# Performance work log

Hardware: AMD Instinct MI355X
Metric: run time of the kernel (lower is better)

The kernel has to match this reference:

```python
import jax, jax.numpy as jnp
import numpy as np

N = 16384
E = 262144
NODE_DIM = 120
NUM_HEADS = 4
NUM_BASIS = 20
MULS = (64, 32, 16)          # multiplicities of 0e, 1e, 2e
LS = (0, 1, 2)
NUM_IRREPS = 112             # 64+32+16
EQUI_DIM = 240               # 64*1 + 32*3 + 16*5
L_MAX = 2
ATTN_DIM_SCALAR = NODE_DIM // NUM_HEADS        # 30
ATTN_DIM_EQUI = NODE_DIM // (L_MAX + 1)        # 40
SCALE_SCALAR = 1.0 / np.sqrt(NODE_DIM)
SCALE_EQUI = 1.0 / np.sqrt(NUM_IRREPS)
EPS = 1e-5

def _blocks():
    off = 0
    for mul, l in zip(MULS, LS):
        d = 2 * l + 1
        yield off, mul, l, d
        off += mul * d

def equi_dot(x):
    # per-irrep self dot: [E, EQUI_DIM] -> [E, NUM_IRREPS] invariants
    outs = []
    for off, mul, l, d in _blocks():
        blk = x[:, off:off + mul * d].reshape(-1, mul, d)
        outs.append(jnp.sum(blk * blk, axis=-1))
    return jnp.concatenate(outs, axis=1)

def gate_to_components(g):
    # broadcast per-irrep scalar gate [E, NUM_IRREPS] to components [E, EQUI_DIM]
    parts = []
    woff = 0
    for mul, l in zip(MULS, LS):
        d = 2 * l + 1
        parts.append(jnp.repeat(g[:, woff:woff + mul, None], d, axis=-1).reshape(-1, mul * d))
        woff += mul
    return jnp.concatenate(parts, axis=1)

def layer_norm(x, w, b):
    mu = jnp.mean(x, -1, keepdims=True)
    var = jnp.var(x, -1, keepdims=True)
    return (x - mu) * jax.lax.rsqrt(var + EPS) * w + b

def o3_layer_norm(x, w):
    # equivariant layer norm: per irrep block, RMS over (mul, components); mean-center l=0 only
    parts = []
    woff = 0
    for off, mul, l, d in _blocks():
        blk = x[:, off:off + mul * d].reshape(-1, mul, d)
        if l == 0:
            blk = blk - jnp.mean(blk, axis=1, keepdims=True)
        rms = jax.lax.rsqrt(jnp.mean(blk * blk, axis=(1, 2), keepdims=True) + EPS)
        blk = blk * rms * w[woff:woff + mul][None, :, None]
        parts.append(blk.reshape(-1, mul * d))
        woff += mul
    return jnp.concatenate(parts, axis=1)

def mlp(x, w1, b1, w2, b2):
    return jax.nn.silu(x @ w1 + b1) @ w2 + b2

def setup_inputs():
    ks = jax.random.split(jax.random.key(0), 24)
    def lin(k, i, o):
        return jax.random.normal(k, (i, o), jnp.float32) / np.sqrt(i)
    return dict(
        node_scalar=jax.random.normal(ks[0], (N, NODE_DIM), jnp.float32),
        node_equi=jax.random.normal(ks[1], (N, EQUI_DIM), jnp.float32),
        rbf=jax.random.normal(ks[2], (E, NUM_BASIS), jnp.float32),
        fcut=jax.random.uniform(ks[3], (E, 1), jnp.float32),
        rsh=jax.random.normal(ks[4], (E, EQUI_DIM), jnp.float32),
        ln_w=jnp.ones((NODE_DIM,), jnp.float32),
        ln_b=jnp.zeros((NODE_DIM,), jnp.float32),
        o3ln_w=jnp.ones((NUM_IRREPS,), jnp.float32),
        Wq=lin(ks[5], NODE_DIM, NODE_DIM),
        Wk=lin(ks[6], NODE_DIM, NODE_DIM),
        Wv=lin(ks[7], NODE_DIM, NODE_DIM),
        Wqs=lin(ks[8], NODE_DIM, NODE_DIM),
        Wks=lin(ks[9], NODE_DIM, NODE_DIM),
        Wvs=lin(ks[10], NODE_DIM, NUM_IRREPS),
        rbf_w1=lin(ks[11], NUM_BASIS, NODE_DIM),
        rbf_b1=jnp.zeros((NODE_DIM,), jnp.float32),
        rbf_w2=lin(ks[12], NODE_DIM, NODE_DIM),
        rbf_b2=jnp.zeros((NODE_DIM,), jnp.float32),
        inv_w1=lin(ks[13], NUM_IRREPS, NODE_DIM),
        inv_b1=jnp.zeros((NODE_DIM,), jnp.float32),
        inv_w2=lin(ks[14], NODE_DIM, NODE_DIM),
        inv_b2=jnp.zeros((NODE_DIM,), jnp.float32),
        edge_index=jax.random.randint(ks[15], (2, E), 0, N),
    )

def reference(node_scalar, node_equi, rbf, fcut, rsh, ln_w, ln_b, o3ln_w, Wq, Wk, Wv, Wqs, Wks, Wvs, rbf_w1, rbf_b1, rbf_w2, rbf_b2, inv_w1, inv_b1, inv_w2, inv_b2, edge_index):
    center, neighbor = edge_index[0], edge_index[1]
    ns = layer_norm(node_scalar, ln_w, ln_b)
    ne = o3_layer_norm(node_equi, o3ln_w)
    q_inv = ns @ Wq; k_inv = ns @ Wk; v_inv = ns @ Wv
    q_sph = ns @ Wqs; k_sph = ns @ Wks; v_sph = ns @ Wvs
    # EquiFilter: equivariant difference -> per-irrep invariants -> MLP, plus radial MLP
    x_ij = ne[neighbor] - ne[center]
    w_ij = mlp(equi_dot(x_ij), inv_w1, inv_b1, inv_w2, inv_b2) + mlp(rbf, rbf_w1, rbf_b1, rbf_w2, rbf_b2)
    w_ij = w_ij * fcut
    # scalar multi-head dot-product attention (softmax-free)
    q_s = (q_inv[center] * w_ij).reshape(E, NUM_HEADS, ATTN_DIM_SCALAR)
    k_s = k_inv[neighbor].reshape(E, NUM_HEADS, ATTN_DIM_SCALAR)
    v_s = v_inv[neighbor].reshape(E, NUM_HEADS, ATTN_DIM_SCALAR)
    attn_s = jnp.sum(q_s * k_s, -1, keepdims=True) * SCALE_SCALAR
    msg_scalar = (attn_s * v_s).reshape(E, NODE_DIM)
    # equivariant gated attention
    q_e = (q_sph[center] * w_ij).reshape(E, L_MAX + 1, ATTN_DIM_EQUI)
    k_e = k_sph[neighbor].reshape(E, L_MAX + 1, ATTN_DIM_EQUI)
    v_e = v_sph[neighbor]                                   # [E, NUM_IRREPS]
    attn_e = jnp.sum(q_e * k_e, -1) * SCALE_EQUI            # [E, L_MAX+1]
    attn_e = jnp.concatenate([jnp.repeat(attn_e[:, i:i + 1], MULS[i], axis=1) for i in range(L_MAX + 1)], axis=1)
    gate = attn_e * v_e                                     # [E, NUM_IRREPS]
    msg_equi = rsh * gate_to_components(gate) * fcut        # elementwise tensor product with 0e gates
    out_scalar = node_scalar.at[center].add(msg_scalar)
    out_equi = node_equi.at[center].add(msg_equi)
    return out_scalar, out_equi
```

## Files before the change

kernel.cpp:

```cpp
#include <hip/hip_runtime.h>
#include <hip/hip_bf16.h>
#include <hip/hip_fp16.h>

#define N_NODES 16384
#define E_EDGES 262144

#define SCALE_S 0.09128709291752768f
#define SCALE_E 0.09449111825230679f

#define OFF_ACC   256
#define ACC_BYTES ((size_t)N_NODES * 360 * 4)
#define OFF_TAB   (OFF_ACC + ACC_BYTES)
#define OFF_NS    (OFF_TAB + (size_t)N_NODES * 952 * 2)
#define OFF_W1T   (OFF_NS + (size_t)N_NODES * 128 * 2)
#define OFF_W2T   (OFF_W1T + 256 * 160 * 2)
#define OFF_WNT   (OFF_W2T + 128 * 256 * 2)
#define OFF_B1    (OFF_WNT + 768 * 128 * 2)
#define OFF_B2    (OFF_B1 + 1024)
#define OFF_WIJ   (OFF_B2 + 512)

#define OFF_CNT   OFF_ACC
#define OFF_BASE  (OFF_ACC + 65536)
#define OFF_CUR   (OFF_ACC + 131584)
#define OFF_SORT  (OFF_ACC + 197632)
#define SORT_CLR_BYTES 197632

typedef __attribute__((ext_vector_type(8))) short short8;
typedef __attribute__((ext_vector_type(4))) float f32x4;

#define SF_STRIDE 168
#define SB_STRIDE 40
#define TR_STRIDE 40

#define REGION1_BYTES (64 * 240 * 2)
#define SMEM_MLP (64 * SF_STRIDE * 2 + REGION1_BYTES + 64 * 4 + 2 * 64 * 4)

static __device__ __forceinline__ float b2f(short s) {
    return __uint_as_float(((unsigned int)(unsigned short)s) << 16);
}
static __device__ __forceinline__ short f2b(float v) {
    __hip_bfloat16 h = __float2bfloat16(v);
    return *reinterpret_cast<short*>(&h);
}
static __device__ __forceinline__ short f2h(float v) {
    __half h = __float2half(v);
    return *reinterpret_cast<short*>(&h);
}
static __device__ __forceinline__ float h2f(short s) {
    __half h = *reinterpret_cast<__half*>(&s);
    return __half2float(h);
}
static __device__ __forceinline__ float ldin(const void* p, size_t i, int bfm) {
    return bfm ? b2f(((const short*)p)[i]) : ((const float*)p)[i];
}
static __device__ __forceinline__ float block_reduce(float v, float* red, int t) {
    __syncthreads();
    red[t] = v;
    __syncthreads();
    for (int s = 128; s > 0; s >>= 1) {
        if (t < s) red[t] += red[t + s];
        __syncthreads();
    }
    return red[0];
}

__global__ void detect_kernel(const unsigned short* __restrict__ lnw_bits, int* __restrict__ flag) {
    if (threadIdx.x == 0 && blockIdx.x == 0)
        *flag = (lnw_bits[0] == 0x3F80u) ? 1 : 0;
}

__global__ __launch_bounds__(256) void hist_kernel(const int* __restrict__ eidx, void* ws) {
    int* cnt = (int*)((char*)ws + OFF_CNT);
    int e = blockIdx.x * 256 + threadIdx.x;
    atomicAdd(&cnt[eidx[e]], 1);
}

__global__ __launch_bounds__(256) void scan_kernel(void* ws) {
    __shared__ int lds[256];
    int* cnt  = (int*)((char*)ws + OFF_CNT);
    int* base = (int*)((char*)ws + OFF_BASE);
    const int t = threadIdx.x;
    int s = 0;
    for (int j = 0; j < 64; ++j) s += cnt[t * 64 + j];
    lds[t] = s;
    __syncthreads();
    for (int off = 1; off < 256; off <<= 1) {
        int add = (t >= off) ? lds[t - off] : 0;
        __syncthreads();
        lds[t] += add;
        __syncthreads();
    }
    int run = lds[t] - s;
    for (int j = 0; j < 64; ++j) {
        int v = cnt[t * 64 + j];
        base[t * 64 + j] = run;
        run += v;
    }
    if (t == 0) base[16384] = E_EDGES;
}

__global__ __launch_bounds__(256) void scatter_kernel(const int* __restrict__ eidx, void* ws) {
    const int* base = (const int*)((char*)ws + OFF_BASE);
    int* cur    = (int*)((char*)ws + OFF_CUR);
    int* sorted = (int*)((char*)ws + OFF_SORT);
    int e = blockIdx.x * 256 + threadIdx.x;
    int c = eidx[e];
    int pos = base[c] + atomicAdd(&cur[c], 1);
    sorted[pos] = e;
}

__global__ __launch_bounds__(256) void prep_kernel(
    const void* inv_w1, const void* rbf_w1, const void* inv_w2, const void* rbf_w2,
    const void* inv_b1, const void* rbf_b1, const void* inv_b2, const void* rbf_b2,
    const void* Wq, const void* Wk, const void* Wv,
    const void* Wqs, const void* Wks, const void* Wvs,
    void* ws, const int* __restrict__ flag)
{
    short* W1T = (short*)((char*)ws + OFF_W1T);
    short* W2T = (short*)((char*)ws + OFF_W2T);
    short* WNT = (short*)((char*)ws + OFF_WNT);
    float* b1c = (float*)((char*)ws + OFF_B1);
    float* b2c = (float*)((char*)ws + OFF_B2);
    const int bfm = *flag;
    int g = blockIdx.x * 256 + threadIdx.x;
    if (g < 40960) {
        int n = g / 160, k = g % 160;
        float v = 0.f;
        if (n < 120 && k < 112) v = ldin(inv_w1, (size_t)k * 120 + n, bfm);
        else if (n >= 120 && n < 240 && k >= 112 && k < 132)
            v = ldin(rbf_w1, (size_t)(k - 112) * 120 + (n - 120), bfm);
        W1T[g] = f2b(v);
    } else if (g < 73728) {
        int g2 = g - 40960;
        int n = g2 / 256, k = g2 % 256;
        float v = 0.f;
        if (n < 120) {
            if (k < 120)      v = ldin(inv_w2, (size_t)k * 120 + n, bfm);
            else if (k < 240) v = ldin(rbf_w2, (size_t)(k - 120) * 120 + n, bfm);
        }
        W2T[g2] = f2b(v);
    } else if (g < 172032) {
        int g3 = g - 73728;
        int n = g3 / 128, k = g3 % 128;
        float v = 0.f;
        if (k < 120) {
            if      (n < 120) v = ldin(Wq,  (size_t)k * 120 + n, bfm);
            else if (n < 240) v = ldin(Wk,  (size_t)k * 120 + (n - 120), bfm);
            else if (n < 360) v = ldin(Wv,  (size_t)k * 120 + (n - 240), bfm);
            else if (n < 480) v = ldin(Wqs, (size_t)k * 120 + (n - 360), bfm);
            else if (n < 600) v = ldin(Wks, (size_t)k * 120 + (n - 480), bfm);
            else if (n < 712) v = ldin(Wvs, (size_t)k * 112 + (n - 600), bfm);
        }
        WNT[g3] = f2b(v);
    } else if (g < 172288) {
        int n = g - 172032;
        b1c[n] = (n < 120) ? ldin(inv_b1, n, bfm) : (n < 240 ? ldin(rbf_b1, n - 120, bfm) : 0.f);
    } else if (g < 172416) {
        int n = g - 172288;
        b2c[n] = (n < 120) ? (ldin(inv_b2, n, bfm) + ldin(rbf_b2, n, bfm)) : 0.f;
    }
}

__global__ __launch_bounds__(256) void nodeln_kernel(
    const void* node_scalar, const void* node_equi,
    const void* ln_w, const void* ln_b, const void* o3ln_w,
    void* ws, const int* __restrict__ flag)
{
    __shared__ float red[256];
    short* NS  = (short*)((char*)ws + OFF_NS);
    short* tab = (short*)((char*)ws + OFF_TAB);
    const int n = blockIdx.x, t = threadIdx.x;
    const int bfm = *flag;

    float xs = 0.f;
    if (t < 120) xs = ldin(node_scalar, (size_t)n * 120 + t, bfm);
    float s  = block_reduce(xs, red, t);
    float s2 = block_reduce(xs * xs, red, t);
    float mean = s * (1.f / 120.f);
    float var  = s2 * (1.f / 120.f) - mean * mean;
    float rstd = rsqrtf(var + 1e-5f);
    float nsv = 0.f;
    if (t < 120) nsv = (xs - mean) * rstd * ldin(ln_w, t, bfm) + ldin(ln_b, t, bfm);
    if (t < 128) NS[(size_t)n * 128 + t] = f2b(t < 120 ? nsv : 0.f);

    float xe = 0.f;
    if (t < 240) xe = ldin(node_equi, (size_t)n * 240 + t, bfm);
    float s0  = block_reduce(t < 64 ? xe : 0.f, red, t);
    float mu0 = s0 * (1.f / 64.f);
    float xc  = (t < 64) ? xe - mu0 : xe;
    float ss0 = block_reduce(t < 64 ? xc * xc : 0.f, red, t);
    float ss1 = block_reduce((t >= 64 && t < 160) ? xe * xe : 0.f, red, t);
    float ss2 = block_reduce((t >= 160 && t < 240) ? xe * xe : 0.f, red, t);
    float r0 = rsqrtf(ss0 * (1.f / 64.f) + 1e-5f);
    float r1 = rsqrtf(ss1 * (1.f / 96.f) + 1e-5f);
    float r2 = rsqrtf(ss2 * (1.f / 80.f) + 1e-5f);
    float nev = 0.f;
    if (t < 64)       nev = xc * r0 * ldin(o3ln_w, t, bfm);
    else if (t < 160) nev = xe * r1 * ldin(o3ln_w, 64 + (t - 64) / 3, bfm);
    else if (t < 240) nev = xe * r2 * ldin(o3ln_w, 96 + (t - 160) / 5, bfm);
    if (t < 240) tab[(size_t)n * 952 + 712 + t] = f2b(nev);
}

__global__ __launch_bounds__(256) void gemm_node_kernel(void* ws)
{
    __shared__ short sA[64 * SB_STRIDE];
    __shared__ short sB[64 * SB_STRIDE];
    const short* NS  = (const short*)((char*)ws + OFF_NS);
    const short* WNT = (const short*)((char*)ws + OFF_WNT);
    short* tab = (short*)((char*)ws + OFF_TAB);

    const int t = threadIdx.x, w = t >> 6, lane = t & 63;
    const int quad = lane >> 4, l15 = lane & 15;
    const int tileM = (blockIdx.x & 255) * 64;
    const int tileN = (blockIdx.x >> 8) * 64;

    f32x4 acc[4];
    for (int i = 0; i < 4; ++i) acc[i] = (f32x4){0.f, 0.f, 0.f, 0.f};

    for (int k0 = 0; k0 < 128; k0 += 32) {
        __syncthreads();
        {
            int row = t >> 2, ch = t & 3;
            *(short8*)&sA[row * SB_STRIDE + ch * 8] =
                *(const short8*)&NS[(size_t)(tileM + row) * 128 + k0 + ch * 8];
            *(short8*)&sB[row * SB_STRIDE + ch * 8] =
                *(const short8*)&WNT[(size_t)(tileN + row) * 128 + k0 + ch * 8];
        }
        __syncthreads();
        short8 a = *(const short8*)&sA[(w * 16 + l15) * SB_STRIDE + quad * 8];
        #pragma unroll
        for (int nt = 0; nt < 4; ++nt) {
            short8 b = *(const short8*)&sB[(nt * 16 + l15) * SB_STRIDE + quad * 8];
            acc[nt] = __builtin_amdgcn_mfma_f32_16x16x32_bf16(a, b, acc[nt], 0, 0, 0);
        }
    }
    #pragma unroll
    for (int nt = 0; nt < 4; ++nt)
        #pragma unroll
        for (int r = 0; r < 4; ++r) {
            int row = tileM + w * 16 + quad * 4 + r;
            int col = tileN + nt * 16 + l15;
            if (col < 712) tab[(size_t)row * 952 + col] = f2b(acc[nt][r]);
        }
}

__global__ __launch_bounds__(256, 3) void mlp_kernel(
    const void* rbf, const void* fcut, const int* __restrict__ eidx,
    void* ws, const int* __restrict__ flag)
{
    extern __shared__ __align__(16) char smem[];
    short* sF   = (short*)smem;
    char*  reg1 = smem + 64 * SF_STRIDE * 2;
    short* sD   = (short*)reg1;
    short* sB   = (short*)reg1;
    short* sTr  = (short*)(reg1 + 256 * SB_STRIDE * 2);
    float* sFc  = (float*)(reg1 + REGION1_BYTES);
    int*   sIC  = (int*)(sFc + 64);
    int*   sIN  = sIC + 64;

    const short* tab = (const short*)((char*)ws + OFF_TAB);
    const short* W1T = (const short*)((char*)ws + OFF_W1T);
    const short* W2T = (const short*)((char*)ws + OFF_W2T);
    const float* b1c = (const float*)((char*)ws + OFF_B1);
    const float* b2c = (const float*)((char*)ws + OFF_B2);
    short* Wij = (short*)((char*)ws + OFF_WIJ);

    const int t = threadIdx.x, w = t >> 6, lane = t & 63;
    const int quad = lane >> 4, l15 = lane & 15;
    const int bfm = *flag;
    const int e0 = blockIdx.x * 64;

    if (t < 64)       sIC[t] = eidx[e0 + t];
    else if (t < 128) sIN[t - 64] = eidx[E_EDGES + e0 + (t - 64)];
    else if (t < 192) sFc[t - 128] = ldin(fcut, e0 + (t - 128), bfm);
    __syncthreads();

    for (int u = t; u < 1920; u += 256) {
        int le = u / 30, ch = u - le * 30;
        const short* pc = tab + (size_t)sIC[le] * 952 + 712 + ch * 8;
        const short* pn = tab + (size_t)sIN[le] * 952 + 712 + ch * 8;
        short8 a = *(const short8*)pc;
        short8 b = *(const short8*)pn;
        short8 s;
        #pragma unroll
        for (int j = 0; j < 8; ++j) {
            float d = b2f(b[j]) - b2f(a[j]);
            s[j] = f2h(d * d);
        }
        *(short8*)&sD[le * 240 + ch * 8] = s;
    }
    __syncthreads();

    for (int u = t; u < 8192; u += 256) {
        int le = u >> 7, ir = u & 127;
        if (ir < 112) {
            const short* p = sD + le * 240;
            float a;
            if (ir < 64) {
                a = h2f(p[ir]);
            } else if (ir < 96) {
                int off = 64 + 3 * (ir - 64);
                a = h2f(p[off]) + h2f(p[off + 1]) + h2f(p[off + 2]);
            } else {
                int off = 160 + 5 * (ir - 96);
                a = h2f(p[off]) + h2f(p[off + 1]) + h2f(p[off + 2])
                  + h2f(p[off + 3]) + h2f(p[off + 4]);
            }
            sF[le * SF_STRIDE + ir] = f2b(a);
        }
    }
    for (int u = t; u < 4096; u += 256) {
        int le = u >> 6, c = u & 63;
        if (c < 48) {
            float v = (c < 20) ? ldin(rbf, (size_t)(e0 + le) * 20 + c, bfm) : 0.f;
            sF[le * SF_STRIDE + 112 + c] = f2b(v);
        }
    }
    __syncthreads();

    f32x4 acc[16];
    #pragma unroll
    for (int i = 0; i < 16; ++i) acc[i] = (f32x4){0.f, 0.f, 0.f, 0.f};
    for (int k0 = 0; k0 < 160; k0 += 32) {
        #pragma unroll
        for (int i = 0; i < 4; ++i) {
            int u = t + i * 256, n = u >> 2, ch = u & 3;
            *(short8*)&sB[n * SB_STRIDE + ch * 8] =
                *(const short8*)&W1T[(size_t)n * 160 + k0 + ch * 8];
        }
        __syncthreads();
        short8 a = *(const short8*)&sF[(w * 16 + l15) * SF_STRIDE + k0 + quad * 8];
        #pragma unroll
        for (int nt = 0; nt < 16; ++nt) {
            short8 b = *(const short8*)&sB[(nt * 16 + l15) * SB_STRIDE + quad * 8];
            acc[nt] = __builtin_amdgcn_mfma_f32_16x16x32_bf16(a, b, acc[nt], 0, 0, 0);
        }
        __syncthreads();
    }

    short* trw = sTr + w * (16 * TR_STRIDE);
    f32x4 acc2[8];
    #pragma unroll
    for (int i = 0; i < 8; ++i) acc2[i] = (f32x4){0.f, 0.f, 0.f, 0.f};
    #pragma unroll
    for (int ks = 0; ks < 8; ++ks) {
        #pragma unroll
        for (int h = 0; h < 2; ++h) {
            int nt = 2 * ks + h;
            float bb = b1c[nt * 16 + l15];
            #pragma unroll
            for (int r = 0; r < 4; ++r) {
                float v = acc[nt][r] + bb;
                v = v / (1.f + __expf(-v));
                trw[(quad * 4 + r) * TR_STRIDE + h * 16 + l15] = f2b(v);
            }
        }
        #pragma unroll
        for (int i = 0; i < 2; ++i) {
            int u = t + i * 256, n = u >> 2, ch = u & 3;
            *(short8*)&sB[n * SB_STRIDE + ch * 8] =
                *(const short8*)&W2T[(size_t)n * 256 + ks * 32 + ch * 8];
        }
        __syncthreads();
        short8 a = *(const short8*)&trw[l15 * TR_STRIDE + quad * 8];
        #pragma unroll
        for (int nt = 0; nt < 8; ++nt) {
            short8 b = *(const short8*)&sB[(nt * 16 + l15) * SB_STRIDE + quad * 8];
            acc2[nt] = __builtin_amdgcn_mfma_f32_16x16x32_bf16(a, b, acc2[nt], 0, 0, 0);
        }
        __syncthreads();
    }

    #pragma unroll
    for (int nt = 0; nt < 8; ++nt)
        #pragma unroll
        for (int r = 0; r < 4; ++r) {
            int lrow = w * 16 + quad * 4 + r;
            int col = nt * 16 + l15;
            float v = (acc2[nt][r] + b2c[col]) * sFc[lrow];
            Wij[(size_t)(e0 + lrow) * 128 + col] = f2b(v);
        }
}

__global__ __launch_bounds__(256) void edge2g_kernel(
    const void* node_scalar, const void* node_equi,
    const void* rsh, const void* fcut, const int* __restrict__ eidx,
    void* ws, void* out, const int* __restrict__ flag)
{
    const short* tab = (const short*)((char*)ws + OFF_TAB);
    const short* Wij = (const short*)((char*)ws + OFF_WIJ);
    const int* base   = (const int*)((char*)ws + OFF_BASE);
    const int* sorted = (const int*)((char*)ws + OFF_SORT);

    const int t = threadIdx.x, wvid = t >> 6, lane = t & 63;
    const int c = blockIdx.x * 4 + wvid;
    const int bfm = *flag;
    const short* tc = tab + (size_t)c * 952;

    const int i16 = lane & 15, g = lane >> 4;
    const int ksa = 30 * g + i16;
    const bool vb = (i16 < 14);
    const int ksb = ksa + 16;
    const int kea = 40 * g + i16;
    const bool ge = (g < 3), gec = ge && (i16 < 8);
    const float qs_a = b2f(tc[ksa]);
    const float qs_b = vb ? b2f(tc[ksb]) : 0.f;
    const float qe_a = ge  ? b2f(tc[360 + kea])      : 0.f;
    const float qe_b = ge  ? b2f(tc[360 + kea + 16]) : 0.f;
    const float qe_c = gec ? b2f(tc[360 + kea + 32]) : 0.f;
    const int bs0 = 16 * (lane / 30);
    const int bs1 = 16 * ((lane + 64) / 30);
    int wi_[4], be_[4];
    bool jv_[4];
    #pragma unroll
    for (int s = 0; s < 4; ++s) {
        int j = lane + 64 * s;
        jv_[s] = (j < 240);
        int wi = 0, le = 0;
        if (j < 64)       { wi = j;                  le = 0; }
        else if (j < 160) { wi = 64 + (j - 64) / 3;  le = 1; }
        else if (j < 240) { wi = 96 + (j - 160) / 5; le = 2; }
        wi_[s] = wi; be_[s] = 16 * le;
    }

    float accS0 = 0.f, accS1 = 0.f;
    float accE0 = 0.f, accE1 = 0.f, accE2 = 0.f, accE3 = 0.f;

    const int b0 = base[c], b1 = base[c + 1];
    for (int p = b0; p < b1; ++p) {
        const int e = sorted[p];
        const int n = eidx[E_EDGES + e];
        const short* tn = tab + (size_t)n * 952;
        const short* wr = Wij + (size_t)e * 128;
        const float fc = ldin(fcut, e, bfm);

        float ps = qs_a * b2f(wr[ksa]) * b2f(tn[120 + ksa])
                 + qs_b * b2f(wr[ksb]) * b2f(tn[120 + ksb]);
        float wv_ea = ge  ? b2f(wr[kea])      : 0.f;
        float wv_eb = ge  ? b2f(wr[kea + 16]) : 0.f;
        float wv_ec = gec ? b2f(wr[kea + 32]) : 0.f;
        float pe = qe_a * wv_ea * b2f(tn[480 + kea])
                 + qe_b * wv_eb * b2f(tn[480 + kea + 16])
                 + qe_c * wv_ec * b2f(tn[480 + kea + 32]);
        #pragma unroll
        for (int m = 1; m < 16; m <<= 1) {
            ps += __shfl_xor(ps, m, 16);
            pe += __shfl_xor(pe, m, 16);
        }
        ps *= SCALE_S;
        pe *= SCALE_E;

        float a0 = __shfl(ps, bs0);
        float a1 = __shfl(ps, bs1);
        accS0 += a0 * b2f(tn[240 + lane]);
        if (lane < 56) accS1 += a1 * b2f(tn[240 + 64 + lane]);

        float ae0 = __shfl(pe, be_[0]);
        float ae1 = __shfl(pe, be_[1]);
        float ae2 = __shfl(pe, be_[2]);
        float ae3 = __shfl(pe, be_[3]);
        accE0 += ae0 * b2f(tn[600 + wi_[0]]) * ldin(rsh, (size_t)e * 240 + lane, bfm) * fc;
        accE1 += ae1 * b2f(tn[600 + wi_[1]]) * ldin(rsh, (size_t)e * 240 + lane + 64, bfm) * fc;
        accE2 += ae2 * b2f(tn[600 + wi_[2]]) * ldin(rsh, (size_t)e * 240 + lane + 128, bfm) * fc;
        if (jv_[3])
            accE3 += ae3 * b2f(tn[600 + wi_[3]]) * ldin(rsh, (size_t)e * 240 + lane + 192, bfm) * fc;
    }

    const size_t so = (size_t)c * 120;
    {
        float v = ldin(node_scalar, so + lane, bfm) + accS0;
        size_t i = so + lane;
        if (bfm) ((short*)out)[i] = f2b(v); else ((float*)out)[i] = v;
    }
    if (lane < 56) {
        float v = ldin(node_scalar, so + 64 + lane, bfm) + accS1;
        size_t i = so + 64 + lane;
        if (bfm) ((short*)out)[i] = f2b(v); else ((float*)out)[i] = v;
    }
    const size_t eo = (size_t)c * 240;
    const size_t ob = (size_t)N_NODES * 120;
    {
        float v = ldin(node_equi, eo + lane, bfm) + accE0;
        size_t i = ob + eo + lane;
        if (bfm) ((short*)out)[i] = f2b(v); else ((float*)out)[i] = v;
    }
    {
        float v = ldin(node_equi, eo + lane + 64, bfm) + accE1;
        size_t i = ob + eo + lane + 64;
        if (bfm) ((short*)out)[i] = f2b(v); else ((float*)out)[i] = v;
    }
    {
        float v = ldin(node_equi, eo + lane + 128, bfm) + accE2;
        size_t i = ob + eo + lane + 128;
        if (bfm) ((short*)out)[i] = f2b(v); else ((float*)out)[i] = v;
    }
    if (jv_[3]) {
        float v = ldin(node_equi, eo + lane + 192, bfm) + accE3;
        size_t i = ob + eo + lane + 192;
        if (bfm) ((short*)out)[i] = f2b(v); else ((float*)out)[i] = v;
    }
}

extern "C" void kernel_launch(void* const* d_in, const int* in_sizes, int n_in,
                              void* d_out, int out_size, void* d_ws, size_t ws_size,
                              hipStream_t stream) {
    const void* node_scalar = d_in[0];
    const void* node_equi   = d_in[1];
    const void* rbf         = d_in[2];
    const void* fcut        = d_in[3];
    const void* rsh         = d_in[4];
    const void* ln_w        = d_in[5];
    const void* ln_b        = d_in[6];
    const void* o3ln_w      = d_in[7];
    const void* Wq          = d_in[8];
    const void* Wk          = d_in[9];
    const void* Wv          = d_in[10];
    const void* Wqs         = d_in[11];
    const void* Wks         = d_in[12];
    const void* Wvs         = d_in[13];
    const void* rbf_w1      = d_in[14];
    const void* rbf_b1      = d_in[15];
    const void* rbf_w2      = d_in[16];
    const void* rbf_b2      = d_in[17];
    const void* inv_w1      = d_in[18];
    const void* inv_b1      = d_in[19];
    const void* inv_w2      = d_in[20];
    const void* inv_b2      = d_in[21];
    const int*  edge_index  = (const int*)d_in[22];

    int* flag = (int*)d_ws;

    hipFuncSetAttribute(reinterpret_cast<const void*>(mlp_kernel),
                        hipFuncAttributeMaxDynamicSharedMemorySize, SMEM_MLP);

    detect_kernel<<<1, 64, 0, stream>>>((const unsigned short*)ln_w, flag);
    hipMemsetAsync((char*)d_ws + OFF_ACC, 0, SORT_CLR_BYTES, stream);

    hist_kernel<<<E_EDGES / 256, 256, 0, stream>>>(edge_index, d_ws);
    scan_kernel<<<1, 256, 0, stream>>>(d_ws);
    scatter_kernel<<<E_EDGES / 256, 256, 0, stream>>>(edge_index, d_ws);

    prep_kernel<<<674, 256, 0, stream>>>(
        inv_w1, rbf_w1, inv_w2, rbf_w2, inv_b1, rbf_b1, inv_b2, rbf_b2,
        Wq, Wk, Wv, Wqs, Wks, Wvs, d_ws, flag);

    nodeln_kernel<<<N_NODES, 256, 0, stream>>>(
        node_scalar, node_equi, ln_w, ln_b, o3ln_w, d_ws, flag);

    gemm_node_kernel<<<256 * 12, 256, 0, stream>>>(d_ws);

    mlp_kernel<<<E_EDGES / 64, 256, SMEM_MLP, stream>>>(
        rbf, fcut, edge_index, d_ws, flag);

    edge2g_kernel<<<N_NODES / 4, 256, 0, stream>>>(
        node_scalar, node_equi, rsh, fcut, edge_index, d_ws, d_out, flag);
}
```

Before: 847.8 us.

## Software-pipeline edge gather loads and use wave-shuffle reductions in node layernorm

The edge aggregation loop now double-buffers per-edge operands in registers. It issues the gathers for the next edge (Wij row, neighbor table entries, rsh, fcut) before computing the current edge, which hides gather latency behind the shuffle-reduction math. The node layer-norm kernel replaces repeated shared-memory tree reductions, each with many barriers, with wave-level xor-shuffle reductions that batch three sums at a time and need only two block barriers. The cost is higher register pressure from the two ER buffers, which may reduce occupancy.

```diff
diff --git a/kernel.cpp b/kernel.cpp
--- a/kernel.cpp
+++ b/kernel.cpp
@@ -52,16 +52,6 @@
 }
 static __device__ __forceinline__ float ldin(const void* p, size_t i, int bfm) {
     return bfm ? b2f(((const short*)p)[i]) : ((const float*)p)[i];
-}
-static __device__ __forceinline__ float block_reduce(float v, float* red, int t) {
-    __syncthreads();
-    red[t] = v;
-    __syncthreads();
-    for (int s = 128; s > 0; s >>= 1) {
-        if (t < s) red[t] += red[t + s];
-        __syncthreads();
-    }
-    return red[0];
 }
 
 __global__ void detect_kernel(const unsigned short* __restrict__ lnw_bits, int* __restrict__ flag) {
@@ -166,31 +156,54 @@
     const void* ln_w, const void* ln_b, const void* o3ln_w,
     void* ws, const int* __restrict__ flag)
 {
-    __shared__ float red[256];
+    __shared__ float sm[24];
     short* NS  = (short*)((char*)ws + OFF_NS);
     short* tab = (short*)((char*)ws + OFF_TAB);
-    const int n = blockIdx.x, t = threadIdx.x;
+    const int n = blockIdx.x, t = threadIdx.x, wv = t >> 6, lane = t & 63;
     const int bfm = *flag;
 
-    float xs = 0.f;
-    if (t < 120) xs = ldin(node_scalar, (size_t)n * 120 + t, bfm);
-    float s  = block_reduce(xs, red, t);
-    float s2 = block_reduce(xs * xs, red, t);
+    float xs = (t < 120) ? ldin(node_scalar, (size_t)n * 120 + t, bfm) : 0.f;
+    float xe = (t < 240) ? ldin(node_equi, (size_t)n * 240 + t, bfm) : 0.f;
+
+    float a = xs, b = xs * xs, c = (t < 64) ? xe : 0.f;
+    #pragma unroll
+    for (int m = 1; m < 64; m <<= 1) {
+        a += __shfl_xor(a, m);
+        b += __shfl_xor(b, m);
+        c += __shfl_xor(c, m);
+    }
+    if (lane == 0) { sm[wv * 3] = a; sm[wv * 3 + 1] = b; sm[wv * 3 + 2] = c; }
+    __syncthreads();
+    float s  = sm[0] + sm[3] + sm[6] + sm[9];
+    float s2 = sm[1] + sm[4] + sm[7] + sm[10];
+    float s0 = sm[2] + sm[5] + sm[8] + sm[11];
+
     float mean = s * (1.f / 120.f);
     float var  = s2 * (1.f / 120.f) - mean * mean;
     float rstd = rsqrtf(var + 1e-5f);
-    float nsv = 0.f;
-    if (t < 120) nsv = (xs - mean) * rstd * ldin(ln_w, t, bfm) + ldin(ln_b, t, bfm);
-    if (t < 128) NS[(size_t)n * 128 + t] = f2b(t < 120 ? nsv : 0.f);
-
-    float xe = 0.f;
-    if (t < 240) xe = ldin(node_equi, (size_t)n * 240 + t, bfm);
-    float s0  = block_reduce(t < 64 ? xe : 0.f, red, t);
+    if (t < 128) {
+        float nsv = 0.f;
+        if (t < 120) nsv = (xs - mean) * rstd * ldin(ln_w, t, bfm) + ldin(ln_b, t, bfm);
+        NS[(size_t)n * 128 + t] = f2b(nsv);
+    }
+
     float mu0 = s0 * (1.f / 64.f);
     float xc  = (t < 64) ? xe - mu0 : xe;
-    float ss0 = block_reduce(t < 64 ? xc * xc : 0.f, red, t);
-    float ss1 = block_reduce((t >= 64 && t < 160) ? xe * xe : 0.f, red, t);
-    float ss2 = block_reduce((t >= 160 && t < 240) ? xe * xe : 0.f, red, t);
+    float p0 = (t < 64) ? xc * xc : 0.f;
+    float p1 = (t >= 64 && t < 160) ? xe * xe : 0.f;
+    float p2 = (t >= 160 && t < 240) ? xe * xe : 0.f;
+    #pragma unroll
+    for (int m = 1; m < 64; m <<= 1) {
+        p0 += __shfl_xor(p0, m);
+        p1 += __shfl_xor(p1, m);
+        p2 += __shfl_xor(p2, m);
+    }
+    if (lane == 0) { sm[12 + wv * 3] = p0; sm[12 + wv * 3 + 1] = p1; sm[12 + wv * 3 + 2] = p2; }
+    __syncthreads();
+    float ss0 = sm[12] + sm[15] + sm[18] + sm[21];
+    float ss1 = sm[13] + sm[16] + sm[19] + sm[22];
+    float ss2 = sm[14] + sm[17] + sm[20] + sm[23];
+
     float r0 = rsqrtf(ss0 * (1.f / 64.f) + 1e-5f);
     float r1 = rsqrtf(ss1 * (1.f / 96.f) + 1e-5f);
     float r2 = rsqrtf(ss2 * (1.f / 80.f) + 1e-5f);
@@ -382,6 +395,13 @@
         }
 }
 
+struct ER {
+    float wsa, wsb, wea, web, wec;
+    float ka, kb, kae, kbe, kce;
+    float v0, v1, vs0, vs1, vs2, vs3;
+    float r0, r1, r2, r3, fc;
+};
+
 __global__ __launch_bounds__(256) void edge2g_kernel(
     const void* node_scalar, const void* node_equi,
     const void* rsh, const void* fcut, const int* __restrict__ eidx,
@@ -410,12 +430,11 @@
     const float qe_c = gec ? b2f(tc[360 + kea + 32]) : 0.f;
     const int bs0 = 16 * (lane / 30);
     const int bs1 = 16 * ((lane + 64) / 30);
+    const bool jv3 = (lane < 48);
     int wi_[4], be_[4];
-    bool jv_[4];
     #pragma unroll
     for (int s = 0; s < 4; ++s) {
         int j = lane + 64 * s;
-        jv_[s] = (j < 240);
         int wi = 0, le = 0;
         if (j < 64)       { wi = j;                  le = 0; }
         else if (j < 160) { wi = 64 + (j - 64) / 3;  le = 1; }
@@ -426,22 +445,37 @@
     float accS0 = 0.f, accS1 = 0.f;
     float accE0 = 0.f, accE1 = 0.f, accE2 = 0.f, accE3 = 0.f;
 
-    const int b0 = base[c], b1 = base[c + 1];
-    for (int p = b0; p < b1; ++p) {
-        const int e = sorted[p];
-        const int n = eidx[E_EDGES + e];
-        const short* tn = tab + (size_t)n * 952;
+    auto loadE = [&](ER& R, int e, int nn) {
+        const short* tn = tab + (size_t)nn * 952;
         const short* wr = Wij + (size_t)e * 128;
-        const float fc = ldin(fcut, e, bfm);
-
-        float ps = qs_a * b2f(wr[ksa]) * b2f(tn[120 + ksa])
-                 + qs_b * b2f(wr[ksb]) * b2f(tn[120 + ksb]);
-        float wv_ea = ge  ? b2f(wr[kea])      : 0.f;
-        float wv_eb = ge  ? b2f(wr[kea + 16]) : 0.f;
-        float wv_ec = gec ? b2f(wr[kea + 32]) : 0.f;
-        float pe = qe_a * wv_ea * b2f(tn[480 + kea])
-                 + qe_b * wv_eb * b2f(tn[480 + kea + 16])
-                 + qe_c * wv_ec * b2f(tn[480 + kea + 32]);
+        R.wsa = b2f(wr[ksa]);
+        R.wsb = b2f(wr[ksb]);
+        R.ka  = b2f(tn[120 + ksa]);
+        R.kb  = b2f(tn[120 + ksb]);
+        if (ge) {
+            R.wea = b2f(wr[kea]);
+            R.web = b2f(wr[kea + 16]);
+            R.wec = b2f(wr[kea + 32]);
+        } else { R.wea = 0.f; R.web = 0.f; R.wec = 0.f; }
+        R.kae = b2f(tn[480 + kea]);
+        R.kbe = b2f(tn[480 + kea + 16]);
+        R.kce = b2f(tn[480 + kea + 32]);
+        R.v0  = b2f(tn[240 + lane]);
+        R.v1  = b2f(tn[304 + lane]);
+        R.vs0 = b2f(tn[600 + wi_[0]]);
+        R.vs1 = b2f(tn[600 + wi_[1]]);
+        R.vs2 = b2f(tn[600 + wi_[2]]);
+        R.vs3 = b2f(tn[600 + wi_[3]]);
+        R.r0  = ldin(rsh, (size_t)e * 240 + lane, bfm);
+        R.r1  = ldin(rsh, (size_t)e * 240 + lane + 64, bfm);
+        R.r2  = ldin(rsh, (size_t)e * 240 + lane + 128, bfm);
+        R.r3  = jv3 ? ldin(rsh, (size_t)e * 240 + lane + 192, bfm) : 0.f;
+        R.fc  = ldin(fcut, e, bfm);
+    };
+
+    auto computeE = [&](const ER& R) {
+        float ps = qs_a * R.wsa * R.ka + qs_b * R.wsb * R.kb;
+        float pe = qe_a * R.wea * R.kae + qe_b * R.web * R.kbe + qe_c * R.wec * R.kce;
         #pragma unroll
         for (int m = 1; m < 16; m <<= 1) {
             ps += __shfl_xor(ps, m, 16);
@@ -449,21 +483,34 @@
         }
         ps *= SCALE_S;
         pe *= SCALE_E;
-
-        float a0 = __shfl(ps, bs0);
-        float a1 = __shfl(ps, bs1);
-        accS0 += a0 * b2f(tn[240 + lane]);
-        if (lane < 56) accS1 += a1 * b2f(tn[240 + 64 + lane]);
-
+        float a0  = __shfl(ps, bs0);
+        float a1  = __shfl(ps, bs1);
         float ae0 = __shfl(pe, be_[0]);
         float ae1 = __shfl(pe, be_[1]);
         float ae2 = __shfl(pe, be_[2]);
         float ae3 = __shfl(pe, be_[3]);
-        accE0 += ae0 * b2f(tn[600 + wi_[0]]) * ldin(rsh, (size_t)e * 240 + lane, bfm) * fc;
-        accE1 += ae1 * b2f(tn[600 + wi_[1]]) * ldin(rsh, (size_t)e * 240 + lane + 64, bfm) * fc;
-        accE2 += ae2 * b2f(tn[600 + wi_[2]]) * ldin(rsh, (size_t)e * 240 + lane + 128, bfm) * fc;
-        if (jv_[3])
-            accE3 += ae3 * b2f(tn[600 + wi_[3]]) * ldin(rsh, (size_t)e * 240 + lane + 192, bfm) * fc;
+        accS0 += a0 * R.v0;
+        if (lane < 56) accS1 += a1 * R.v1;
+        float fr = R.fc;
+        accE0 += ae0 * R.vs0 * R.r0 * fr;
+        accE1 += ae1 * R.vs1 * R.r1 * fr;
+        accE2 += ae2 * R.vs2 * R.r2 * fr;
+        if (jv3) accE3 += ae3 * R.vs3 * R.r3 * fr;
+    };
+
+    const int b0v = base[c], b1v = base[c + 1];
+    if (b0v < b1v) {
+        ER A, B;
+        { int e = sorted[b0v]; int nn = eidx[E_EDGES + e]; loadE(A, e, nn); }
+        int p = b0v;
+        while (true) {
+            if (p + 1 < b1v) { int e = sorted[p + 1]; int nn = eidx[E_EDGES + e]; loadE(B, e, nn); }
+            computeE(A);
+            ++p; if (p >= b1v) break;
+            if (p + 1 < b1v) { int e = sorted[p + 1]; int nn = eidx[E_EDGES + e]; loadE(A, e, nn); }
+            computeE(B);
+            ++p; if (p >= b1v) break;
+        }
     }
 
     const size_t so = (size_t)c * 120;
@@ -494,7 +541,7 @@
         size_t i = ob + eo + lane + 128;
         if (bfm) ((short*)out)[i] = f2b(v); else ((float*)out)[i] = v;
     }
-    if (jv_[3]) {
+    if (jv3) {
         float v = ldin(node_equi, eo + lane + 192, bfm) + accE3;
         size_t i = ob + eo + lane + 192;
         if (bfm) ((short*)out)[i] = f2b(v); else ((float*)out)[i] = v;
```

Result: faster. 830.1 us (-2.1%).
